# Kernel optimization log

Measured on AMD Instinct MI355X. Metric: run time of the kernel, lower is better.

## Reference

```python
import jax, jax.numpy as jnp
import numpy as np

# --- physics constants (from source) ---
T_STALL = 5.4 * (1.0 / 100.0)
W_FREE = 1620.0 * (1.0 / 60.0) * 2.0 * np.pi
L_X = 0.129907
L_Y = 0.095724
A = L_X + L_Y
R = 4 * 0.0254
MASS = 6.0
INERTIA = MASS
MOMENT_OF_INERTIA = MASS * (12 * 0.0254) ** 2 / 6.0

LV2WV = np.array([[1, -1, -A], [1, 1, A], [1, 1, -A], [1, -1, A]], dtype=np.float32) / R  # [4,3]
CD2MD = np.array([[1, -1, -1], [1, 1, 1], [1, 1, -1], [1, -1, 1]], dtype=np.float32)      # [4,3]
WT2LA = (LV2WV.T / np.array([INERTIA, INERTIA, MOMENT_OF_INERTIA], dtype=np.float32)[:, None]).astype(np.float32)  # [3,4]

BATCH = 4_000_000


def _rot(c, s):
    # builds [..., 3, 3] = [[c,-s,0],[s,c,0],[0,0,1]]
    z = jnp.zeros_like(c)
    o = jnp.ones_like(c)
    return jnp.stack([
        jnp.stack([c, -s, z], axis=-1),
        jnp.stack([s, c, z], axis=-1),
        jnp.stack([z, z, o], axis=-1),
    ], axis=-2)


def setup_inputs() -> dict:
    key = jax.random.key(0)
    k1, k2 = jax.random.split(key)
    state = jax.random.normal(k1, (BATCH, 6), dtype=jnp.float32)
    control_duty = jax.random.normal(k2, (3,), dtype=jnp.float32)
    t = jnp.zeros((1,), dtype=jnp.float32)
    return {"t": t, "state": state, "control_duty": control_duty}


def reference(t, state, control_duty):
    lv2wv = jnp.asarray(LV2WV)
    cd2md = jnp.asarray(CD2MD)
    wt2la = jnp.asarray(WT2LA)

    absolute_vel = state[..., 3:]            # [..., 3]
    theta = state[..., 2]                    # [...]

    # absolute -> local frame
    a2l = _rot(jnp.cos(-theta), jnp.sin(-theta))                      # [...,3,3]
    local_vel = jnp.einsum('...ij,...j->...i', a2l, absolute_vel)     # [...,3]
    wheel_vel = jnp.einsum('ij,...j->...i', lv2wv, local_vel)         # [...,4]

    motor_duty = cd2md @ control_duty                                 # [4]
    is_same_direction = (jnp.sign(motor_duty * wheel_vel) + 1.0) / 2.0
    wheel_torque = T_STALL * (1.0 - jnp.abs(wheel_vel) * is_same_direction / W_FREE) * motor_duty  # [...,4]

    local_accel = jnp.einsum('ij,...j->...i', wt2la, wheel_torque)    # [...,3]

    # local -> absolute frame
    l2a = _rot(jnp.cos(theta), jnp.sin(theta))
    absolute_accel = jnp.einsum('...ij,...j->...i', l2a, local_accel)

    return jnp.concatenate([absolute_vel, absolute_accel], axis=-1)   # [...,6]
```

## Files before the change

kernel.cpp:

```cpp
#include <hip/hip_runtime.h>
#include <math.h>

namespace k {
constexpr double dA     = 0.129907 + 0.095724;
constexpr double dR     = 4.0 * 0.0254;
constexpr double dI     = 6.0;
constexpr double dMOI   = 6.0 * (12.0 * 0.0254) * (12.0 * 0.0254) / 6.0;
constexpr float T_STALL   = (float)(5.4 / 100.0);
constexpr float INV_WFREE = (float)(1.0 / (1620.0 / 60.0 * 2.0 * 3.14159265358979323846));
constexpr float A         = (float)dA;
constexpr float INV_R     = (float)(1.0 / dR);
constexpr float INV_RI    = (float)(1.0 / (dR * dI));
constexpr float A_RMOI    = (float)(dA / (dR * dMOI));
}

typedef float f32x4 __attribute__((ext_vector_type(4)));

__device__ __forceinline__ float wheel_torque(float w, float m) {
    float p = m * w;
    float sgn = (float)(p > 0.0f) - (float)(p < 0.0f);
    float isd = 0.5f * (sgn + 1.0f);
    return k::T_STALL * (1.0f - fabsf(w) * isd * k::INV_WFREE) * m;
}

__device__ __forceinline__ void mecanum_elem(const float st[6],
                                             float m0, float m1, float m2, float m3,
                                             float o[6]) {
    float theta = st[2];
    float s, c;
    sincosf(theta, &s, &c);

    float v0 = st[3], v1 = st[4], v2 = st[5];

    float lv0 = c * v0 + s * v1;
    float lv1 = c * v1 - s * v0;

    float al2 = k::A * v2;
    float w0 = (lv0 - lv1 - al2) * k::INV_R;
    float w1 = (lv0 + lv1 + al2) * k::INV_R;
    float w2 = (lv0 + lv1 - al2) * k::INV_R;
    float w3 = (lv0 - lv1 + al2) * k::INV_R;

    float t0 = wheel_torque(w0, m0);
    float t1 = wheel_torque(w1, m1);
    float t2 = wheel_torque(w2, m2);
    float t3 = wheel_torque(w3, m3);

    float la0 = (t0 + t1 + t2 + t3) * k::INV_RI;
    float la1 = (-t0 + t1 + t2 - t3) * k::INV_RI;
    float la2 = (-t0 + t1 - t2 + t3) * k::A_RMOI;

    float aa0 = c * la0 - s * la1;
    float aa1 = s * la0 + c * la1;

    o[0] = st[3]; o[1] = st[4]; o[2] = st[5];
    o[3] = aa0; o[4] = aa1; o[5] = la2;
}

#define PAIRS_PER_BLOCK 256
#define F4_PER_BLOCK    (PAIRS_PER_BLOCK * 3)

__global__ __launch_bounds__(256, 8) void mecanum_wave_kernel(
    const float4* __restrict__ state4,
    const float* __restrict__ cd,
    float4* __restrict__ out4,
    int n_pairs) {
    __shared__ float4 s[F4_PER_BLOCK];

    const int tid  = threadIdx.x;
    const int wave = tid >> 6;
    const int lane = tid & 63;
    const int pair_base = blockIdx.x * PAIRS_PER_BLOCK;
    const int f4_base   = pair_base * 3;
    const int total4    = n_pairs * 3;
    const int ws = wave * 192;

    float u0 = cd[0], u1 = cd[1], u2 = cd[2];
    float m0 = u0 - u1 - u2;
    float m1 = u0 + u1 + u2;
    float m2 = u0 + u1 - u2;
    float m3 = u0 - u1 + u2;

#pragma unroll
    for (int r = 0; r < 3; ++r) {
        int g = f4_base + ws + r * 64 + lane;
        if (g < total4) s[ws + r * 64 + lane] = state4[g];
    }
    __builtin_amdgcn_wave_barrier();
    asm volatile("" ::: "memory");

    if (pair_base + wave * 64 + lane < n_pairs) {
        float4 a  = s[ws + 3 * lane + 0];
        float4 b  = s[ws + 3 * lane + 1];
        float4 g4 = s[ws + 3 * lane + 2];

        float stA[6] = { a.x, a.y, a.z, a.w, b.x, b.y };
        float stB[6] = { b.z, b.w, g4.x, g4.y, g4.z, g4.w };
        float oA[6], oB[6];
        mecanum_elem(stA, m0, m1, m2, m3, oA);
        mecanum_elem(stB, m0, m1, m2, m3, oB);

        s[ws + 3 * lane + 0] = make_float4(oA[0], oA[1], oA[2], oA[3]);
        s[ws + 3 * lane + 1] = make_float4(oA[4], oA[5], oB[0], oB[1]);
        s[ws + 3 * lane + 2] = make_float4(oB[2], oB[3], oB[4], oB[5]);
    }
    __builtin_amdgcn_wave_barrier();
    asm volatile("" ::: "memory");

#pragma unroll
    for (int r = 0; r < 3; ++r) {
        int idx = ws + r * 64 + lane;
        int g = f4_base + idx;
        if (g < total4) {
            f32x4 v;
            float4 t = s[idx];
            v.x = t.x; v.y = t.y; v.z = t.z; v.w = t.w;
            __builtin_nontemporal_store(v, (f32x4*)&out4[g]);
        }
    }
}

__global__ void mecanum_tail_kernel(const float* __restrict__ state,
                                    const float* __restrict__ cd,
                                    float* __restrict__ out,
                                    int start, int n) {
    int i = start + blockIdx.x * blockDim.x + threadIdx.x;
    if (i >= n) return;
    float u0 = cd[0], u1 = cd[1], u2 = cd[2];
    float m0 = u0 - u1 - u2;
    float m1 = u0 + u1 + u2;
    float m2 = u0 + u1 - u2;
    float m3 = u0 - u1 + u2;
    float st[6], o[6];
#pragma unroll
    for (int j = 0; j < 6; ++j) st[j] = state[6 * i + j];
    mecanum_elem(st, m0, m1, m2, m3, o);
#pragma unroll
    for (int j = 0; j < 6; ++j) out[6 * i + j] = o[j];
}

extern "C" void kernel_launch(void* const* d_in, const int* in_sizes, int n_in,
                              void* d_out, int out_size, void* d_ws, size_t ws_size,
                              hipStream_t stream) {
    const float* state = (const float*)d_in[1];
    const float* cd    = (const float*)d_in[2];
    float* out         = (float*)d_out;

    int n = in_sizes[1] / 6;
    int n_pairs = n / 2;

    if (n_pairs > 0) {
        int grid = (n_pairs + PAIRS_PER_BLOCK - 1) / PAIRS_PER_BLOCK;
        mecanum_wave_kernel<<<grid, 256, 0, stream>>>(
            (const float4*)state, cd, (float4*)out, n_pairs);
    }
    if (n & 1) {
        mecanum_tail_kernel<<<1, 64, 0, stream>>>(state, cd, out, 2 * n_pairs, n);
    }
}
```

Measured before the change: 175.0 us.

## Use persistent grid-stride blocks with register prefetch and double-buffered LDS

Replaces the one-tile-per-block launch with a persistent grid capped at 1536 blocks, each looping over tiles. While computing the current tile, each wave loads the next tile into registers, then writes it into a second LDS buffer after storing the current output. The goal is to overlap global load latency with compute and stores and to cut block launch overhead. The cost is higher register and LDS pressure, with the occupancy hint lowered from 8 to 6, which may hurt latency hiding in this memory-bound kernel.

```diff
diff --git a/kernel.cpp b/kernel.cpp
--- a/kernel.cpp
+++ b/kernel.cpp
@@ -59,21 +59,25 @@
 
 #define PAIRS_PER_BLOCK 256
 #define F4_PER_BLOCK    (PAIRS_PER_BLOCK * 3)
-
-__global__ __launch_bounds__(256, 8) void mecanum_wave_kernel(
+#define GRID_BLOCKS     1536
+
+__global__ __launch_bounds__(256, 6) void mecanum_pipe_kernel(
     const float4* __restrict__ state4,
     const float* __restrict__ cd,
     float4* __restrict__ out4,
     int n_pairs) {
-    __shared__ float4 s[F4_PER_BLOCK];
+    __shared__ float4 s[2][F4_PER_BLOCK];
 
     const int tid  = threadIdx.x;
     const int wave = tid >> 6;
     const int lane = tid & 63;
-    const int pair_base = blockIdx.x * PAIRS_PER_BLOCK;
-    const int f4_base   = pair_base * 3;
-    const int total4    = n_pairs * 3;
-    const int ws = wave * 192;
+    const int ws   = wave * 192;
+    const int total4 = n_pairs * 3;
+    const int ntiles = (n_pairs + PAIRS_PER_BLOCK - 1) / PAIRS_PER_BLOCK;
+    const int stride = gridDim.x;
+
+    int tp = blockIdx.x;
+    if (tp >= ntiles) return;
 
     float u0 = cd[0], u1 = cd[1], u2 = cd[2];
     float m0 = u0 - u1 - u2;
@@ -81,42 +85,77 @@
     float m2 = u0 + u1 - u2;
     float m3 = u0 - u1 + u2;
 
-#pragma unroll
-    for (int r = 0; r < 3; ++r) {
-        int g = f4_base + ws + r * 64 + lane;
-        if (g < total4) s[ws + r * 64 + lane] = state4[g];
+    {
+        const int fb = tp * F4_PER_BLOCK + ws;
+#pragma unroll
+        for (int r = 0; r < 3; ++r) {
+            int g = fb + r * 64 + lane;
+            float4 v = (g < total4) ? state4[g] : make_float4(0.f, 0.f, 0.f, 0.f);
+            s[0][ws + r * 64 + lane] = v;
+        }
     }
     __builtin_amdgcn_wave_barrier();
     asm volatile("" ::: "memory");
 
-    if (pair_base + wave * 64 + lane < n_pairs) {
-        float4 a  = s[ws + 3 * lane + 0];
-        float4 b  = s[ws + 3 * lane + 1];
-        float4 g4 = s[ws + 3 * lane + 2];
-
-        float stA[6] = { a.x, a.y, a.z, a.w, b.x, b.y };
-        float stB[6] = { b.z, b.w, g4.x, g4.y, g4.z, g4.w };
-        float oA[6], oB[6];
-        mecanum_elem(stA, m0, m1, m2, m3, oA);
-        mecanum_elem(stB, m0, m1, m2, m3, oB);
-
-        s[ws + 3 * lane + 0] = make_float4(oA[0], oA[1], oA[2], oA[3]);
-        s[ws + 3 * lane + 1] = make_float4(oA[4], oA[5], oB[0], oB[1]);
-        s[ws + 3 * lane + 2] = make_float4(oB[2], oB[3], oB[4], oB[5]);
-    }
-    __builtin_amdgcn_wave_barrier();
-    asm volatile("" ::: "memory");
-
-#pragma unroll
-    for (int r = 0; r < 3; ++r) {
-        int idx = ws + r * 64 + lane;
-        int g = f4_base + idx;
-        if (g < total4) {
-            f32x4 v;
-            float4 t = s[idx];
-            v.x = t.x; v.y = t.y; v.z = t.z; v.w = t.w;
-            __builtin_nontemporal_store(v, (f32x4*)&out4[g]);
-        }
+    int cur = 0;
+    while (true) {
+        const int tnext = tp + stride;
+        const bool have_next = tnext < ntiles;
+
+        float4 n0, n1, n2;
+        if (have_next) {
+            const int fb = tnext * F4_PER_BLOCK + ws;
+            int g0 = fb + 0 * 64 + lane;
+            int g1 = fb + 1 * 64 + lane;
+            int g2 = fb + 2 * 64 + lane;
+            n0 = (g0 < total4) ? state4[g0] : make_float4(0.f, 0.f, 0.f, 0.f);
+            n1 = (g1 < total4) ? state4[g1] : make_float4(0.f, 0.f, 0.f, 0.f);
+            n2 = (g2 < total4) ? state4[g2] : make_float4(0.f, 0.f, 0.f, 0.f);
+        }
+
+        if (tp * PAIRS_PER_BLOCK + wave * 64 + lane < n_pairs) {
+            float4 a  = s[cur][ws + 3 * lane + 0];
+            float4 b  = s[cur][ws + 3 * lane + 1];
+            float4 g4 = s[cur][ws + 3 * lane + 2];
+
+            float stA[6] = { a.x, a.y, a.z, a.w, b.x, b.y };
+            float stB[6] = { b.z, b.w, g4.x, g4.y, g4.z, g4.w };
+            float oA[6], oB[6];
+            mecanum_elem(stA, m0, m1, m2, m3, oA);
+            mecanum_elem(stB, m0, m1, m2, m3, oB);
+
+            s[cur][ws + 3 * lane + 0] = make_float4(oA[0], oA[1], oA[2], oA[3]);
+            s[cur][ws + 3 * lane + 1] = make_float4(oA[4], oA[5], oB[0], oB[1]);
+            s[cur][ws + 3 * lane + 2] = make_float4(oB[2], oB[3], oB[4], oB[5]);
+        }
+        __builtin_amdgcn_wave_barrier();
+        asm volatile("" ::: "memory");
+
+        {
+            const int fb = tp * F4_PER_BLOCK;
+#pragma unroll
+            for (int r = 0; r < 3; ++r) {
+                int idx = ws + r * 64 + lane;
+                int g = fb + idx;
+                if (g < total4) {
+                    float4 t = s[cur][idx];
+                    f32x4 v;
+                    v.x = t.x; v.y = t.y; v.z = t.z; v.w = t.w;
+                    __builtin_nontemporal_store(v, (f32x4*)&out4[g]);
+                }
+            }
+        }
+
+        if (!have_next) break;
+
+        s[cur ^ 1][ws + 0 * 64 + lane] = n0;
+        s[cur ^ 1][ws + 1 * 64 + lane] = n1;
+        s[cur ^ 1][ws + 2 * 64 + lane] = n2;
+        __builtin_amdgcn_wave_barrier();
+        asm volatile("" ::: "memory");
+
+        cur ^= 1;
+        tp = tnext;
     }
 }
 
@@ -150,8 +189,9 @@
     int n_pairs = n / 2;
 
     if (n_pairs > 0) {
-        int grid = (n_pairs + PAIRS_PER_BLOCK - 1) / PAIRS_PER_BLOCK;
-        mecanum_wave_kernel<<<grid, 256, 0, stream>>>(
+        int ntiles = (n_pairs + PAIRS_PER_BLOCK - 1) / PAIRS_PER_BLOCK;
+        int grid = ntiles < GRID_BLOCKS ? ntiles : GRID_BLOCKS;
+        mecanum_pipe_kernel<<<grid, 256, 0, stream>>>(
             (const float4*)state, cd, (float4*)out, n_pairs);
     }
     if (n & 1) {
```

Measured after the change: 176.7 us. About the same (+1.0%).
